# Performance work log

Measured on AMD Instinct MI355X. Metric: run time of the kernel, lower is better.

The kernel has to match this reference:

```python
import jax, jax.numpy as jnp
import numpy as np

LAMBDA_OTDL = 1.0


def _emd2_1d(p, q):
    """Exact EMD^2 (squared-distance cost on integer grid) between two 1D
    histograms p, q of length D. For convex cost |i-j|^2 on a line the optimal
    plan is the monotone (quantile) coupling, so
      EMD2 = int_0^1 (F_p^{-1}(t) - F_q^{-1}(t))^2 dt,
    matching ot.emd2 with M[i,j] = |i-j|^2 exactly."""
    D = p.shape[0]
    cp = jnp.cumsum(p)
    cq = jnp.cumsum(q)
    t = jnp.sort(jnp.concatenate([cp, cq]))          # [2D] merged CDF breakpoints
    dt = jnp.diff(t, prepend=jnp.zeros((1,), t.dtype))
    tm = t - 0.5 * dt                                 # segment midpoints
    ip = jnp.clip(jnp.searchsorted(cp, tm, side='left'), 0, D - 1)
    iq = jnp.clip(jnp.searchsorted(cq, tm, side='left'), 0, D - 1)
    return jnp.sum(dt * (ip - iq).astype(p.dtype) ** 2)


def setup_inputs() -> dict:
    key = jax.random.key(0)
    k1, k2 = jax.random.split(key)
    B, C, D, W = 65536, 1, 256, 1
    P = jax.random.uniform(k1, (B, C, D, W), dtype=jnp.float32)
    Q = jax.random.uniform(k2, (B, C, D, W), dtype=jnp.float32)
    return {"P": P, "Q": Q}


def reference(P, Q):
    B = P.shape[0]
    P_prime = P / jnp.sum(P, axis=(2, 3), keepdims=True)
    Q_prime = Q / jnp.sum(Q, axis=(2, 3), keepdims=True)
    p_flat = P_prime.reshape(B, -1)   # [B, D] since C=W=1
    q_flat = Q_prime.reshape(B, -1)
    OT_values = jax.vmap(_emd2_1d)(p_flat, q_flat)          # [B]
    OT_values = jax.lax.stop_gradient(OT_values)            # original detaches (numpy solver)
    mse_loss = jnp.mean((P - Q) ** 2, axis=(1, 2, 3))       # [B]
    loss = mse_loss + LAMBDA_OTDL * OT_values
    return jnp.mean(loss)
```

## Files before the change

kernel.cpp:

```cpp
#include <hip/hip_runtime.h>


#define NW    4
#define DSZ   256
#define LROW  260

template <int CTRL, int RMASK, bool BC>
__device__ __forceinline__ float dpp_add(float x) {
    int t = __builtin_amdgcn_update_dpp(0, __float_as_int(x), CTRL, RMASK, 0xf, BC);
    return x + __int_as_float(t);
}

__device__ __forceinline__ float wave_scan(float x) {
    x = dpp_add<0x111, 0xf, true >(x);
    x = dpp_add<0x112, 0xf, true >(x);
    x = dpp_add<0x114, 0xf, true >(x);
    x = dpp_add<0x118, 0xf, true >(x);
    x = dpp_add<0x142, 0xa, false>(x);
    x = dpp_add<0x143, 0xc, false>(x);
    return x;
}

__device__ __forceinline__ float lane63(float x) {
    return __int_as_float(__builtin_amdgcn_readlane(__float_as_int(x), 63));
}

__global__ __launch_bounds__(256, 8) void otdl_main(
    const float* __restrict__ P, const float* __restrict__ Q,
    double* __restrict__ partial, int B, int bpw)
{
    __shared__ float  s_cp[NW][2][LROW];
    __shared__ float  s_cq[NW][2][LROW];
    __shared__ double s_bsum[NW];

    const int tid  = threadIdx.x;
    const int wv   = tid >> 6;
    const int lane = tid & 63;
    const int wgl  = blockIdx.x * NW + wv;

    float* cpA = s_cp[wv][0];
    float* cqA = s_cq[wv][0];
    float* cpB = s_cp[wv][1];
    float* cqB = s_cq[wv][1];

    if (lane == 0) {
        cpA[DSZ] = 2.0f; cqA[DSZ] = 2.0f;
        cpB[DSZ] = 2.0f; cqB[DSZ] = 2.0f;
    }

    double acc = 0.0;
    const int  k0      = lane * 8;
    const int  npair   = bpw >> 1;
    const long rowbase = (long)wgl * bpw;
    const bool is63    = (lane == 63);

    float4 pv0, qv0, pv1, qv1, np0, nq0, np1, nq1;
    {
        long c0 = (rowbase     < B) ? rowbase     : (B - 1);
        long c1 = (rowbase + 1 < B) ? rowbase + 1 : (B - 1);
        pv0 = reinterpret_cast<const float4*>(P + c0 * DSZ)[lane];
        qv0 = reinterpret_cast<const float4*>(Q + c0 * DSZ)[lane];
        pv1 = reinterpret_cast<const float4*>(P + c1 * DSZ)[lane];
        qv1 = reinterpret_cast<const float4*>(Q + c1 * DSZ)[lane];
    }

    for (int p = 0; p < npair; ++p) {
        long b = rowbase + 2 * p;

        float dx0 = pv0.x - qv0.x, dy0 = pv0.y - qv0.y;
        float dz0 = pv0.z - qv0.z, dw0 = pv0.w - qv0.w;
        float msel0 = dx0*dx0 + dy0*dy0 + dz0*dz0 + dw0*dw0;
        float dx1 = pv1.x - qv1.x, dy1 = pv1.y - qv1.y;
        float dz1 = pv1.z - qv1.z, dw1 = pv1.w - qv1.w;
        float msel1 = dx1*dx1 + dy1*dy1 + dz1*dz1 + dw1*dw1;

        float pl0 = pv0.x + pv0.y + pv0.z + pv0.w;
        float ql0 = qv0.x + qv0.y + qv0.z + qv0.w;
        float pl1 = pv1.x + pv1.y + pv1.z + pv1.w;
        float ql1 = qv1.x + qv1.y + qv1.z + qv1.w;

        float ps0 = wave_scan(pl0);
        float qs0 = wave_scan(ql0);
        float ps1 = wave_scan(pl1);
        float qs1 = wave_scan(ql1);

        float rp0 = __builtin_amdgcn_rcpf(lane63(ps0));
        float rq0 = __builtin_amdgcn_rcpf(lane63(qs0));
        float rp1 = __builtin_amdgcn_rcpf(lane63(ps1));
        float rq1 = __builtin_amdgcn_rcpf(lane63(qs1));
        float pe0 = ps0 - pl0, qe0 = qs0 - ql0;
        float pe1 = ps1 - pl1, qe1 = qs1 - ql1;

        float4 wP0 = make_float4((pe0 + pv0.x) * rp0,
                                 (pe0 + pv0.x + pv0.y) * rp0,
                                 (pe0 + pv0.x + pv0.y + pv0.z) * rp0,
                                 ps0 * rp0);
        float4 wQ0 = make_float4((qe0 + qv0.x) * rq0,
                                 (qe0 + qv0.x + qv0.y) * rq0,
                                 (qe0 + qv0.x + qv0.y + qv0.z) * rq0,
                                 qs0 * rq0);
        float4 wP1 = make_float4((pe1 + pv1.x) * rp1,
                                 (pe1 + pv1.x + pv1.y) * rp1,
                                 (pe1 + pv1.x + pv1.y + pv1.z) * rp1,
                                 ps1 * rp1);
        float4 wQ1 = make_float4((qe1 + qv1.x) * rq1,
                                 (qe1 + qv1.x + qv1.y) * rq1,
                                 (qe1 + qv1.x + qv1.y + qv1.z) * rq1,
                                 qs1 * rq1);

        asm volatile("s_waitcnt lgkmcnt(0)" ::: "memory");

        *reinterpret_cast<float4*>(&cpA[lane * 4]) = wP0;
        *reinterpret_cast<float4*>(&cqA[lane * 4]) = wQ0;
        *reinterpret_cast<float4*>(&cpB[lane * 4]) = wP1;
        *reinterpret_cast<float4*>(&cqB[lane * 4]) = wQ1;

        asm volatile("s_waitcnt lgkmcnt(0)" ::: "memory");

        if (p + 1 < npair) {
            long c0 = (b + 2 < B) ? b + 2 : (B - 1);
            long c1 = (b + 3 < B) ? b + 3 : (B - 1);
            np0 = reinterpret_cast<const float4*>(P + c0 * DSZ)[lane];
            nq0 = reinterpret_cast<const float4*>(Q + c0 * DSZ)[lane];
            np1 = reinterpret_cast<const float4*>(P + c1 * DSZ)[lane];
            nq1 = reinterpret_cast<const float4*>(Q + c1 * DSZ)[lane];
        }

        int lo0 = k0 > DSZ ? k0 - DSZ : 0;
        int hi0 = k0 < DSZ ? k0 : DSZ;
        int lo1 = lo0, hi1 = hi0;
#pragma unroll
        for (int s = 0; s < 9; ++s) {
            int mid0 = (lo0 + hi0) >> 1;
            int mid1 = (lo1 + hi1) >> 1;
            int jm0 = k0 - 1 - mid0;
            int jm1 = k0 - 1 - mid1;
            int jr0 = jm0 < 0 ? 0 : jm0;
            int jr1 = jm1 < 0 ? 0 : jm1;
            float q0 = cqA[jr0];
            float c0 = cpA[mid0];
            float q1 = cqB[jr1];
            float c1 = cpB[mid1];
            bool pr0 = (jm0 < 0) || (q0 <= c0);
            bool pr1 = (jm1 < 0) || (q1 <= c1);
            hi0 = pr0 ? mid0 : hi0;  lo0 = pr0 ? lo0 : mid0 + 1;
            hi1 = pr1 ? mid1 : hi1;  lo1 = pr1 ? lo1 : mid1 + 1;
        }

        const float* pA0 = cpA + lo0;
        const float* pB0 = cqA + (k0 - lo0);
        const float* pA1 = cpB + lo1;
        const float* pB1 = cqB + (k0 - lo1);
        float u0 = (float)(4 * lo0 - 2 * k0 - 1);
        float u1 = (float)(4 * lo1 - 2 * k0 - 1);
        float a0 = pA0[0], c0 = pB0[0], an0 = pA0[1], cn0 = pB0[1];
        float a1 = pA1[0], c1 = pB1[0], an1 = pA1[1], cn1 = pB1[1];
        float e0 = 0.0f, e1 = 0.0f;
#pragma unroll
        for (int s = 0; s < 8; ++s) {
            bool  ea0  = a0 < c0;
            bool  ea1  = a1 < c1;
            float val0 = ea0 ? a0 : c0;
            float val1 = ea1 ? a1 : c1;
            float u20  = u0 + 2.0f;
            float u21  = u1 + 2.0f;
            float cf0  = ea0 ? -u20 : u0;
            float cf1  = ea1 ? -u21 : u1;
            e0 = fmaf(val0, cf0, e0);
            e1 = fmaf(val1, cf1, e1);
            u0 = ea0 ? u20 : (u0 - 2.0f);
            u1 = ea1 ? u21 : (u1 - 2.0f);
            pA0 += ea0 ? 1 : 0;  pB0 += ea0 ? 0 : 1;
            pA1 += ea1 ? 1 : 0;  pB1 += ea1 ? 0 : 1;
            a0 = ea0 ? an0 : a0;  c0 = ea0 ? c0 : cn0;
            a1 = ea1 ? an1 : a1;  c1 = ea1 ? c1 : cn1;
            an0 = pA0[1];  cn0 = pB0[1];
            an1 = pA1[1];  cn1 = pB1[1];
        }

        e0 -= is63 ? fabsf(wP0.w - wQ0.w) : 0.0f;
        e1 -= is63 ? fabsf(wP1.w - wQ1.w) : 0.0f;

        if (b     < B) acc += (double)(e0 + msel0 * (1.0f / 256.0f));
        if (b + 1 < B) acc += (double)(e1 + msel1 * (1.0f / 256.0f));
        pv0 = np0; qv0 = nq0;
        pv1 = np1; qv1 = nq1;
    }

#pragma unroll
    for (int off = 32; off; off >>= 1) {
        double o = __shfl_xor(acc, off, 64);
        acc += o;
    }
    if (lane == 0) s_bsum[wv] = acc;
    __syncthreads();
    if (tid == 0) {
        partial[blockIdx.x] = s_bsum[0] + s_bsum[1] + s_bsum[2] + s_bsum[3];
    }
}

__global__ __launch_bounds__(256) void otdl_reduce(
    const double* __restrict__ partial, int n, float* __restrict__ out, double invB)
{
    __shared__ double sdata[256];
    double a = 0.0;
    for (int i = threadIdx.x; i < n; i += 256) a += partial[i];
    sdata[threadIdx.x] = a;
    __syncthreads();
    for (int s2 = 128; s2 > 0; s2 >>= 1) {
        if (threadIdx.x < s2) sdata[threadIdx.x] += sdata[threadIdx.x + s2];
        __syncthreads();
    }
    if (threadIdx.x == 0) out[0] = (float)(sdata[0] * invB);
}

extern "C" void kernel_launch(void* const* d_in, const int* in_sizes, int n_in,
                              void* d_out, int out_size, void* d_ws, size_t ws_size,
                              hipStream_t stream)
{
    const float* P = (const float*)d_in[0];
    const float* Q = (const float*)d_in[1];
    float* out = (float*)d_out;
    double* partial = (double*)d_ws;

    int B = in_sizes[0] / DSZ;
    const int blocks = 2048;
    const int totalWaves = blocks * NW;
    int bpw = (B + totalWaves - 1) / totalWaves;

    otdl_main<<<blocks, 256, 0, stream>>>(P, Q, partial, B, bpw);
    otdl_reduce<<<1, 256, 0, stream>>>(partial, blocks, out, 1.0 / (double)B);
}
```

Before: 45.72 us.

## Software-pipeline CDF build with merge using double-buffered LDS

Moves the per-row CDF scan, normalisation and LDS store for the next pair of rows into a separate stage. That stage runs before the merge-path EMD computation of the current pair, using a double-buffered LDS layout indexed by iteration parity. Global loads are issued two pairs ahead, and the explicit lgkmcnt waits are dropped. The aim is to overlap scan and DPP work with the LDS-bound merge loop. The cost is twice the LDS per block and a lower launch_bounds occupancy hint (4 instead of 8), which may reduce latency hiding across waves.

```diff
diff --git a/kernel.cpp b/kernel.cpp
--- a/kernel.cpp
+++ b/kernel.cpp
@@ -25,12 +25,39 @@
     return __int_as_float(__builtin_amdgcn_readlane(__float_as_int(x), 63));
 }
 
-__global__ __launch_bounds__(256, 8) void otdl_main(
+__device__ __forceinline__ float fe_stage(const float4 pv, const float4 qv,
+                                          float* cp, float* cq, int lane) {
+    float dx = pv.x - qv.x, dy = pv.y - qv.y;
+    float dz = pv.z - qv.z, dw = pv.w - qv.w;
+    float msel = dx*dx + dy*dy + dz*dz + dw*dw;
+
+    float pl = pv.x + pv.y + pv.z + pv.w;
+    float ql = qv.x + qv.y + qv.z + qv.w;
+    float ps = wave_scan(pl);
+    float qs = wave_scan(ql);
+    float rp = __builtin_amdgcn_rcpf(lane63(ps));
+    float rq = __builtin_amdgcn_rcpf(lane63(qs));
+    float pe = ps - pl, qe = qs - ql;
+
+    float4 wP = make_float4((pe + pv.x) * rp,
+                            (pe + pv.x + pv.y) * rp,
+                            (pe + pv.x + pv.y + pv.z) * rp,
+                            ps * rp);
+    float4 wQ = make_float4((qe + qv.x) * rq,
+                            (qe + qv.x + qv.y) * rq,
+                            (qe + qv.x + qv.y + qv.z) * rq,
+                            qs * rq);
+    *reinterpret_cast<float4*>(&cp[lane * 4]) = wP;
+    *reinterpret_cast<float4*>(&cq[lane * 4]) = wQ;
+    return msel;
+}
+
+__global__ __launch_bounds__(256, 4) void otdl_main(
     const float* __restrict__ P, const float* __restrict__ Q,
     double* __restrict__ partial, int B, int bpw)
 {
-    __shared__ float  s_cp[NW][2][LROW];
-    __shared__ float  s_cq[NW][2][LROW];
+    __shared__ float  s_cp[NW][2][2][LROW];
+    __shared__ float  s_cq[NW][2][2][LROW];
     __shared__ double s_bsum[NW];
 
     const int tid  = threadIdx.x;
@@ -38,14 +65,14 @@
     const int lane = tid & 63;
     const int wgl  = blockIdx.x * NW + wv;
 
-    float* cpA = s_cp[wv][0];
-    float* cqA = s_cq[wv][0];
-    float* cpB = s_cp[wv][1];
-    float* cqB = s_cq[wv][1];
-
     if (lane == 0) {
-        cpA[DSZ] = 2.0f; cqA[DSZ] = 2.0f;
-        cpB[DSZ] = 2.0f; cqB[DSZ] = 2.0f;
+#pragma unroll
+        for (int bf = 0; bf < 2; ++bf)
+#pragma unroll
+            for (int r = 0; r < 2; ++r) {
+                s_cp[wv][bf][r][DSZ] = 2.0f;
+                s_cq[wv][bf][r][DSZ] = 2.0f;
+            }
     }
 
     double acc = 0.0;
@@ -54,7 +81,7 @@
     const long rowbase = (long)wgl * bpw;
     const bool is63    = (lane == 63);
 
-    float4 pv0, qv0, pv1, qv1, np0, nq0, np1, nq1;
+    float4 pv0, qv0, pv1, qv1;
     {
         long c0 = (rowbase     < B) ? rowbase     : (B - 1);
         long c1 = (rowbase + 1 < B) ? rowbase + 1 : (B - 1);
@@ -64,67 +91,41 @@
         qv1 = reinterpret_cast<const float4*>(Q + c1 * DSZ)[lane];
     }
 
+    float mselC0 = fe_stage(pv0, qv0, s_cp[wv][0][0], s_cq[wv][0][0], lane);
+    float mselC1 = fe_stage(pv1, qv1, s_cp[wv][0][1], s_cq[wv][0][1], lane);
+    if (npair > 1) {
+        long bb = rowbase + 2;
+        long c0 = (bb     < B) ? bb     : (B - 1);
+        long c1 = (bb + 1 < B) ? bb + 1 : (B - 1);
+        pv0 = reinterpret_cast<const float4*>(P + c0 * DSZ)[lane];
+        qv0 = reinterpret_cast<const float4*>(Q + c0 * DSZ)[lane];
+        pv1 = reinterpret_cast<const float4*>(P + c1 * DSZ)[lane];
+        qv1 = reinterpret_cast<const float4*>(Q + c1 * DSZ)[lane];
+    }
+
+#pragma unroll 2
     for (int p = 0; p < npair; ++p) {
-        long b = rowbase + 2 * p;
-
-        float dx0 = pv0.x - qv0.x, dy0 = pv0.y - qv0.y;
-        float dz0 = pv0.z - qv0.z, dw0 = pv0.w - qv0.w;
-        float msel0 = dx0*dx0 + dy0*dy0 + dz0*dz0 + dw0*dw0;
-        float dx1 = pv1.x - qv1.x, dy1 = pv1.y - qv1.y;
-        float dz1 = pv1.z - qv1.z, dw1 = pv1.w - qv1.w;
-        float msel1 = dx1*dx1 + dy1*dy1 + dz1*dz1 + dw1*dw1;
-
-        float pl0 = pv0.x + pv0.y + pv0.z + pv0.w;
-        float ql0 = qv0.x + qv0.y + qv0.z + qv0.w;
-        float pl1 = pv1.x + pv1.y + pv1.z + pv1.w;
-        float ql1 = qv1.x + qv1.y + qv1.z + qv1.w;
-
-        float ps0 = wave_scan(pl0);
-        float qs0 = wave_scan(ql0);
-        float ps1 = wave_scan(pl1);
-        float qs1 = wave_scan(ql1);
-
-        float rp0 = __builtin_amdgcn_rcpf(lane63(ps0));
-        float rq0 = __builtin_amdgcn_rcpf(lane63(qs0));
-        float rp1 = __builtin_amdgcn_rcpf(lane63(ps1));
-        float rq1 = __builtin_amdgcn_rcpf(lane63(qs1));
-        float pe0 = ps0 - pl0, qe0 = qs0 - ql0;
-        float pe1 = ps1 - pl1, qe1 = qs1 - ql1;
-
-        float4 wP0 = make_float4((pe0 + pv0.x) * rp0,
-                                 (pe0 + pv0.x + pv0.y) * rp0,
-                                 (pe0 + pv0.x + pv0.y + pv0.z) * rp0,
-                                 ps0 * rp0);
-        float4 wQ0 = make_float4((qe0 + qv0.x) * rq0,
-                                 (qe0 + qv0.x + qv0.y) * rq0,
-                                 (qe0 + qv0.x + qv0.y + qv0.z) * rq0,
-                                 qs0 * rq0);
-        float4 wP1 = make_float4((pe1 + pv1.x) * rp1,
-                                 (pe1 + pv1.x + pv1.y) * rp1,
-                                 (pe1 + pv1.x + pv1.y + pv1.z) * rp1,
-                                 ps1 * rp1);
-        float4 wQ1 = make_float4((qe1 + qv1.x) * rq1,
-                                 (qe1 + qv1.x + qv1.y) * rq1,
-                                 (qe1 + qv1.x + qv1.y + qv1.z) * rq1,
-                                 qs1 * rq1);
-
-        asm volatile("s_waitcnt lgkmcnt(0)" ::: "memory");
-
-        *reinterpret_cast<float4*>(&cpA[lane * 4]) = wP0;
-        *reinterpret_cast<float4*>(&cqA[lane * 4]) = wQ0;
-        *reinterpret_cast<float4*>(&cpB[lane * 4]) = wP1;
-        *reinterpret_cast<float4*>(&cqB[lane * 4]) = wQ1;
-
-        asm volatile("s_waitcnt lgkmcnt(0)" ::: "memory");
-
+        const int cur = p & 1;
+
+        float mselN0 = 0.0f, mselN1 = 0.0f;
         if (p + 1 < npair) {
-            long c0 = (b + 2 < B) ? b + 2 : (B - 1);
-            long c1 = (b + 3 < B) ? b + 3 : (B - 1);
-            np0 = reinterpret_cast<const float4*>(P + c0 * DSZ)[lane];
-            nq0 = reinterpret_cast<const float4*>(Q + c0 * DSZ)[lane];
-            np1 = reinterpret_cast<const float4*>(P + c1 * DSZ)[lane];
-            nq1 = reinterpret_cast<const float4*>(Q + c1 * DSZ)[lane];
-        }
+            mselN0 = fe_stage(pv0, qv0, s_cp[wv][cur ^ 1][0], s_cq[wv][cur ^ 1][0], lane);
+            mselN1 = fe_stage(pv1, qv1, s_cp[wv][cur ^ 1][1], s_cq[wv][cur ^ 1][1], lane);
+        }
+        if (p + 2 < npair) {
+            long bb = rowbase + 2 * (p + 2);
+            long c0 = (bb     < B) ? bb     : (B - 1);
+            long c1 = (bb + 1 < B) ? bb + 1 : (B - 1);
+            pv0 = reinterpret_cast<const float4*>(P + c0 * DSZ)[lane];
+            qv0 = reinterpret_cast<const float4*>(Q + c0 * DSZ)[lane];
+            pv1 = reinterpret_cast<const float4*>(P + c1 * DSZ)[lane];
+            qv1 = reinterpret_cast<const float4*>(Q + c1 * DSZ)[lane];
+        }
+
+        const float* cpA = s_cp[wv][cur][0];
+        const float* cqA = s_cq[wv][cur][0];
+        const float* cpB = s_cp[wv][cur][1];
+        const float* cqB = s_cq[wv][cur][1];
 
         int lo0 = k0 > DSZ ? k0 - DSZ : 0;
         int hi0 = k0 < DSZ ? k0 : DSZ;
@@ -178,13 +179,14 @@
             an1 = pA1[1];  cn1 = pB1[1];
         }
 
-        e0 -= is63 ? fabsf(wP0.w - wQ0.w) : 0.0f;
-        e1 -= is63 ? fabsf(wP1.w - wQ1.w) : 0.0f;
-
-        if (b     < B) acc += (double)(e0 + msel0 * (1.0f / 256.0f));
-        if (b + 1 < B) acc += (double)(e1 + msel1 * (1.0f / 256.0f));
-        pv0 = np0; qv0 = nq0;
-        pv1 = np1; qv1 = nq1;
+        e0 -= is63 ? fabsf(cpA[DSZ - 1] - cqA[DSZ - 1]) : 0.0f;
+        e1 -= is63 ? fabsf(cpB[DSZ - 1] - cqB[DSZ - 1]) : 0.0f;
+
+        long b = rowbase + 2 * p;
+        if (b     < B) acc += (double)(e0 + mselC0 * (1.0f / 256.0f));
+        if (b + 1 < B) acc += (double)(e1 + mselC1 * (1.0f / 256.0f));
+        mselC0 = mselN0;
+        mselC1 = mselN1;
     }
 
 #pragma unroll
```

Measured after the change: 43.58 us. 1.05x faster.
